# Kernel optimization log

Hardware: AMD Instinct MI355X
Metric: run time of the kernel (lower is better)

Reference implementation:

```python
import jax, jax.numpy as jnp
import numpy as np

B, F, D = 4096, 32, 32
LAYER_SIZE = [128, 128]


def setup_inputs() -> dict:
    key = jax.random.key(0)
    k1, k2, k3 = jax.random.split(key, 3)
    inputs = jax.random.normal(k1, (B, F, D), dtype=jnp.float32)
    # CIN filters: shape [1, field_nums[0]*field_nums[i], field_nums[i+1]]
    field_nums = [F] + LAYER_SIZE
    filter_0 = (jax.random.normal(k2, (1, field_nums[0] * field_nums[0], field_nums[1]), dtype=jnp.float32) * 0.05)
    filter_1 = (jax.random.normal(k3, (1, field_nums[0] * field_nums[1], field_nums[2]), dtype=jnp.float32) * 0.05)
    return {"inputs": inputs, "filter_0": filter_0, "filter_1": filter_1}


def _cin_forward(inputs, filters):
    x0 = inputs          # [B, F, D] -- hidden_nn_layers[0]
    prev = inputs        # hidden_nn_layers[-1]
    outs = []
    for W in filters:    # W: [1, F*M, N]
        # outer product over field dims: [B, F, M, D]
        z = jnp.einsum('bhd,bmd->bhmd', x0, prev)
        b, h, m, d = z.shape
        z = z.reshape(b, h * m, d)                 # [B, F*M, D]
        # 1x1 conv over the F*M axis == contraction with W[0]: [F*M, N]
        cur = jnp.einsum('bpd,pn->bnd', z, W[0])   # [B, N, D]
        cur = jax.nn.relu(cur)
        prev = cur
        outs.append(cur)
    result = jnp.concatenate(outs, axis=1)         # [B, sum(layer_size), D]
    return jnp.sum(result, axis=-1)                # [B, sum(layer_size)]


def reference(inputs, filter_0, filter_1):
    return _cin_forward(inputs, (filter_0, filter_1))
```

## Files before the change

kernel.cpp:

```cpp
#include <hip/hip_runtime.h>


typedef _Float16 half_t;
typedef _Float16 half4v __attribute__((ext_vector_type(4)));
typedef _Float16 half8 __attribute__((ext_vector_type(8)));
typedef float f32x16 __attribute__((ext_vector_type(16)));

__global__ void prep_w_kernel(const float* __restrict__ W0,
                              const float* __restrict__ W1,
                              half_t* __restrict__ Wp0,
                              half_t* __restrict__ Wp1) {
  int gid = blockIdx.x * 256 + threadIdx.x;
  int n = gid & 127;
  int tg = (gid >> 7) & 1;
  int s = gid >> 8;
  const float* W;
  half_t* Wp;
  int M, sl;
  if (s < 64) { W = W0; Wp = Wp0; M = 32; sl = s; }
  else        { W = W1; Wp = Wp1; M = 128; sl = s - 64; }
  int h = sl & 31, mc = sl >> 5;
  int kbase = h * M + mc * 16 + tg * 8;
  half8 v;
#pragma unroll
  for (int j = 0; j < 8; ++j) v[j] = (half_t)W[(size_t)(kbase + j) * 128 + n];
  *(half8*)(Wp + ((size_t)(sl * 2 + tg) * 128 + n) * 8) = v;
}

__device__ __forceinline__ int pswz(int row, int m) {
  return row * 128 + (((m >> 3) ^ (row & 15)) << 3) + (m & 7);
}

__device__ __forceinline__ f32x16 mfma3216(half8 a, half8 b, f32x16 c) {
  return __builtin_amdgcn_mfma_f32_32x32x16_f16(a, b, c, 0, 0, 0);
}

template <int MC, bool L1>
__device__ __forceinline__ void layer_loop(const half_t* __restrict__ Wp,
                                           const half_t* __restrict__ psrc,
                                           const half_t* __restrict__ xQb,
                                           int woff, int l31, int hi,
                                           f32x16 acc[8]) {
  half8 P[8];
#pragma unroll
  for (int rt = 0; rt < 8; ++rt)
    P[rt] = L1 ? *(const half8*)&psrc[(rt * 32 + l31) * 40 + hi * 8]
               : *(const half8*)&psrc[pswz(rt * 32 + l31, hi * 8)];

  half8 Br0 = *(const half8*)(Wp + (size_t)0 * 2048 + woff);
  half8 Br1 = *(const half8*)(Wp + (size_t)1 * 2048 + woff);
  half8 Br2 = *(const half8*)(Wp + (size_t)2 * 2048 + woff);
  half8 Br3 = *(const half8*)(Wp + (size_t)3 * 2048 + woff);

#pragma unroll 1
  for (int mc = 0; mc < MC; ++mc) {
#pragma unroll 1
    for (int p = 0; p < 8; ++p) {
      const int h0 = p * 4;
      const int sb = mc * 32 + h0;
      half8 xq0 = *(const half8*)(xQb + (h0 + 0) * 256);
      half8 xq1 = *(const half8*)(xQb + (h0 + 1) * 256);
      half8 xq2 = *(const half8*)(xQb + (h0 + 2) * 256);
      half8 xq3 = *(const half8*)(xQb + (h0 + 3) * 256);

#define SSTEP(XQ, BR, OFFJ)                                               \
  {                                                                       \
    half8 A0 = P[0] * XQ[0], A1 = P[1] * XQ[1], A2 = P[2] * XQ[2],        \
          A3 = P[3] * XQ[3];                                              \
    acc[0] = mfma3216(A0, BR, acc[0]);                                    \
    acc[1] = mfma3216(A1, BR, acc[1]);                                    \
    acc[2] = mfma3216(A2, BR, acc[2]);                                    \
    acc[3] = mfma3216(A3, BR, acc[3]);                                    \
    half8 A4 = P[4] * XQ[4], A5 = P[5] * XQ[5], A6 = P[6] * XQ[6],        \
          A7 = P[7] * XQ[7];                                              \
    acc[4] = mfma3216(A4, BR, acc[4]);                                    \
    acc[5] = mfma3216(A5, BR, acc[5]);                                    \
    acc[6] = mfma3216(A6, BR, acc[6]);                                    \
    acc[7] = mfma3216(A7, BR, acc[7]);                                    \
    BR = *(const half8*)(Wp +                                             \
                         (size_t)((sb + 4 + OFFJ) & (MC * 32 - 1)) * 2048 \
                         + woff);                                         \
  }
      SSTEP(xq0, Br0, 0)
      SSTEP(xq1, Br1, 1)
      SSTEP(xq2, Br2, 2)
      SSTEP(xq3, Br3, 3)
#undef SSTEP
    }
    if (mc + 1 < MC) {
      const int mn = (mc + 1) * 16;
#pragma unroll
      for (int rt = 0; rt < 8; ++rt)
        P[rt] = L1 ? *(const half8*)&psrc[(rt * 32 + l31) * 40 + mn + hi * 8]
                   : *(const half8*)&psrc[pswz(rt * 32 + l31, mn + hi * 8)];
    }
  }
}

__global__ __launch_bounds__(256, 2) void cin_fused_kernel(
    const float* __restrict__ x0,
    const half_t* __restrict__ Wp0,
    const half_t* __restrict__ Wp1,
    float* __restrict__ out) {
  __shared__ half_t xQ[32 * 32 * 8];
  __shared__ half_t prevT[8 * 32 * 128];
  half_t* xT = prevT;

  const int tid = threadIdx.x;
  const int b0 = blockIdx.x * 8;

  const float4* x4 = (const float4*)(x0 + (size_t)b0 * 1024);
#pragma unroll
  for (int r = 0; r < 8; ++r) {
    int q = r * 256 + tid;
    float4 v = x4[q];
    int e4 = q * 4;
    int bi = e4 >> 10, h = (e4 >> 5) & 31, d0 = e4 & 31;
    half4v hv = {(half_t)v.x, (half_t)v.y, (half_t)v.z, (half_t)v.w};
#pragma unroll
    for (int j = 0; j < 4; ++j) {
      xQ[(h * 32 + d0 + j) * 8 + bi] = hv[j];
      xT[(bi * 32 + d0 + j) * 40 + h] = hv[j];
    }
  }
  __syncthreads();

  const int lane = tid & 63;
  const int l31 = lane & 31;
  const int hi = lane >> 5;
  const int wave = tid >> 6;

  const int woff = hi * 1024 + (wave * 32 + l31) * 8;
  const half_t* xQb = xQ + l31 * 8;

  f32x16 acc[8];
#pragma unroll
  for (int rt = 0; rt < 8; ++rt)
#pragma unroll
    for (int r = 0; r < 16; ++r) acc[rt][r] = 0.f;

  layer_loop<2, true>(Wp0, xT, xQb, woff, l31, hi, acc);

  __syncthreads();

#pragma unroll
  for (int rt = 0; rt < 8; ++rt) {
    float s = 0.f;
#pragma unroll
    for (int r = 0; r < 16; ++r) {
      float v = acc[rt][r];
      v = v > 0.f ? v : 0.f;
      s += v;
      int d = (r & 3) + ((r >> 2) << 3) + hi * 4;
      prevT[pswz(rt * 32 + d, wave * 32 + l31)] = (half_t)v;
      acc[rt][r] = 0.f;
    }
    s += __shfl_down(s, 32);
    if (lane < 32)
      out[(size_t)(b0 + rt) * 256 + wave * 32 + lane] = s;
  }
  __syncthreads();

  layer_loop<8, false>(Wp1, prevT, xQb, woff, l31, hi, acc);

#pragma unroll
  for (int rt = 0; rt < 8; ++rt) {
    float s = 0.f;
#pragma unroll
    for (int r = 0; r < 16; ++r) {
      float v = acc[rt][r];
      s += v > 0.f ? v : 0.f;
    }
    s += __shfl_down(s, 32);
    if (lane < 32)
      out[(size_t)(b0 + rt) * 256 + 128 + wave * 32 + lane] = s;
  }
}

extern "C" void kernel_launch(void* const* d_in, const int* in_sizes, int n_in,
                              void* d_out, int out_size, void* d_ws,
                              size_t ws_size, hipStream_t stream) {
  const float* x0 = (const float*)d_in[0];
  const float* w0 = (const float*)d_in[1];
  const float* w1 = (const float*)d_in[2];
  float* out = (float*)d_out;
  char* ws = (char*)d_ws;

  half_t* Wp0 = (half_t*)(ws);
  half_t* Wp1 = (half_t*)(ws + 64 * 2048 * 2);

  hipLaunchKernelGGL(prep_w_kernel, dim3(320), dim3(256), 0, stream, w0, w1,
                     Wp0, Wp1);
  hipLaunchKernelGGL(cin_fused_kernel, dim3(512), dim3(256), 0, stream, x0,
                     Wp0, Wp1, out);
}
```

Before: 204.1 us.

## Shrink per-block batch tile from 8 to 2 samples and raise occupancy

Each block now processes 2 batch rows instead of 8, with 4x more blocks and a launch bound targeting 4 blocks per CU. The xQ shared layout is repacked so one half8 load supplies the x0 values for four fields across both batch rows. This cuts registers and LDS per block to improve occupancy and latency hiding. The cost is 4x less reuse of each loaded weight fragment, so global/L2 weight traffic per MFMA rises sharply.

```diff
diff --git a/kernel.cpp b/kernel.cpp
--- a/kernel.cpp
+++ b/kernel.cpp
@@ -40,12 +40,12 @@
                                            const half_t* __restrict__ psrc,
                                            const half_t* __restrict__ xQb,
                                            int woff, int l31, int hi,
-                                           f32x16 acc[8]) {
-  half8 P[8];
+                                           f32x16 acc[2]) {
+  half8 P[2];
 #pragma unroll
-  for (int rt = 0; rt < 8; ++rt)
-    P[rt] = L1 ? *(const half8*)&psrc[(rt * 32 + l31) * 40 + hi * 8]
-               : *(const half8*)&psrc[pswz(rt * 32 + l31, hi * 8)];
+  for (int bi = 0; bi < 2; ++bi)
+    P[bi] = L1 ? *(const half8*)&psrc[(bi * 32 + l31) * 40 + hi * 8]
+               : *(const half8*)&psrc[pswz(bi * 32 + l31, hi * 8)];
 
   half8 Br0 = *(const half8*)(Wp + (size_t)0 * 2048 + woff);
   half8 Br1 = *(const half8*)(Wp + (size_t)1 * 2048 + woff);
@@ -56,62 +56,50 @@
   for (int mc = 0; mc < MC; ++mc) {
 #pragma unroll 1
     for (int p = 0; p < 8; ++p) {
-      const int h0 = p * 4;
-      const int sb = mc * 32 + h0;
-      half8 xq0 = *(const half8*)(xQb + (h0 + 0) * 256);
-      half8 xq1 = *(const half8*)(xQb + (h0 + 1) * 256);
-      half8 xq2 = *(const half8*)(xQb + (h0 + 2) * 256);
-      half8 xq3 = *(const half8*)(xQb + (h0 + 3) * 256);
+      const int sb = mc * 32 + 4 * p;
+      half8 xq = *(const half8*)(xQb + p * 256);
 
-#define SSTEP(XQ, BR, OFFJ)                                               \
-  {                                                                       \
-    half8 A0 = P[0] * XQ[0], A1 = P[1] * XQ[1], A2 = P[2] * XQ[2],        \
-          A3 = P[3] * XQ[3];                                              \
-    acc[0] = mfma3216(A0, BR, acc[0]);                                    \
-    acc[1] = mfma3216(A1, BR, acc[1]);                                    \
-    acc[2] = mfma3216(A2, BR, acc[2]);                                    \
-    acc[3] = mfma3216(A3, BR, acc[3]);                                    \
-    half8 A4 = P[4] * XQ[4], A5 = P[5] * XQ[5], A6 = P[6] * XQ[6],        \
-          A7 = P[7] * XQ[7];                                              \
-    acc[4] = mfma3216(A4, BR, acc[4]);                                    \
-    acc[5] = mfma3216(A5, BR, acc[5]);                                    \
-    acc[6] = mfma3216(A6, BR, acc[6]);                                    \
-    acc[7] = mfma3216(A7, BR, acc[7]);                                    \
-    BR = *(const half8*)(Wp +                                             \
-                         (size_t)((sb + 4 + OFFJ) & (MC * 32 - 1)) * 2048 \
-                         + woff);                                         \
+#define SSTEP(J, BR)                                                       \
+  {                                                                        \
+    half8 A0 = P[0] * xq[J * 2 + 0];                                       \
+    half8 A1 = P[1] * xq[J * 2 + 1];                                       \
+    acc[0] = mfma3216(A0, BR, acc[0]);                                     \
+    acc[1] = mfma3216(A1, BR, acc[1]);                                     \
+    BR = *(const half8*)(Wp +                                              \
+                         (size_t)((sb + 4 + J) & (MC * 32 - 1)) * 2048 +   \
+                         woff);                                            \
   }
-      SSTEP(xq0, Br0, 0)
-      SSTEP(xq1, Br1, 1)
-      SSTEP(xq2, Br2, 2)
-      SSTEP(xq3, Br3, 3)
+      SSTEP(0, Br0)
+      SSTEP(1, Br1)
+      SSTEP(2, Br2)
+      SSTEP(3, Br3)
 #undef SSTEP
     }
     if (mc + 1 < MC) {
       const int mn = (mc + 1) * 16;
 #pragma unroll
-      for (int rt = 0; rt < 8; ++rt)
-        P[rt] = L1 ? *(const half8*)&psrc[(rt * 32 + l31) * 40 + mn + hi * 8]
-                   : *(const half8*)&psrc[pswz(rt * 32 + l31, mn + hi * 8)];
+      for (int bi = 0; bi < 2; ++bi)
+        P[bi] = L1 ? *(const half8*)&psrc[(bi * 32 + l31) * 40 + mn + hi * 8]
+                   : *(const half8*)&psrc[pswz(bi * 32 + l31, mn + hi * 8)];
     }
   }
 }
 
-__global__ __launch_bounds__(256, 2) void cin_fused_kernel(
+__global__ __launch_bounds__(256, 4) void cin_fused_kernel(
     const float* __restrict__ x0,
     const half_t* __restrict__ Wp0,
     const half_t* __restrict__ Wp1,
     float* __restrict__ out) {
-  __shared__ half_t xQ[32 * 32 * 8];
-  __shared__ half_t prevT[8 * 32 * 128];
+  __shared__ half_t xQ[8 * 32 * 8];
+  __shared__ half_t prevT[2 * 32 * 128];
   half_t* xT = prevT;
 
   const int tid = threadIdx.x;
-  const int b0 = blockIdx.x * 8;
+  const int b0 = blockIdx.x * 2;
 
   const float4* x4 = (const float4*)(x0 + (size_t)b0 * 1024);
 #pragma unroll
-  for (int r = 0; r < 8; ++r) {
+  for (int r = 0; r < 2; ++r) {
     int q = r * 256 + tid;
     float4 v = x4[q];
     int e4 = q * 4;
@@ -119,7 +107,7 @@
     half4v hv = {(half_t)v.x, (half_t)v.y, (half_t)v.z, (half_t)v.w};
 #pragma unroll
     for (int j = 0; j < 4; ++j) {
-      xQ[(h * 32 + d0 + j) * 8 + bi] = hv[j];
+      xQ[((h >> 2) * 32 + d0 + j) * 8 + (h & 3) * 2 + bi] = hv[j];
       xT[(bi * 32 + d0 + j) * 40 + h] = hv[j];
     }
   }
@@ -133,47 +121,47 @@
   const int woff = hi * 1024 + (wave * 32 + l31) * 8;
   const half_t* xQb = xQ + l31 * 8;
 
-  f32x16 acc[8];
+  f32x16 acc[2];
 #pragma unroll
-  for (int rt = 0; rt < 8; ++rt)
+  for (int bi = 0; bi < 2; ++bi)
 #pragma unroll
-    for (int r = 0; r < 16; ++r) acc[rt][r] = 0.f;
+    for (int r = 0; r < 16; ++r) acc[bi][r] = 0.f;
 
   layer_loop<2, true>(Wp0, xT, xQb, woff, l31, hi, acc);
 
   __syncthreads();
 
 #pragma unroll
-  for (int rt = 0; rt < 8; ++rt) {
+  for (int bi = 0; bi < 2; ++bi) {
     float s = 0.f;
 #pragma unroll
     for (int r = 0; r < 16; ++r) {
-      float v = acc[rt][r];
+      float v = acc[bi][r];
       v = v > 0.f ? v : 0.f;
       s += v;
       int d = (r & 3) + ((r >> 2) << 3) + hi * 4;
-      prevT[pswz(rt * 32 + d, wave * 32 + l31)] = (half_t)v;
-      acc[rt][r] = 0.f;
+      prevT[pswz(bi * 32 + d, wave * 32 + l31)] = (half_t)v;
+      acc[bi][r] = 0.f;
     }
     s += __shfl_down(s, 32);
     if (lane < 32)
-      out[(size_t)(b0 + rt) * 256 + wave * 32 + lane] = s;
+      out[(size_t)(b0 + bi) * 256 + wave * 32 + lane] = s;
   }
   __syncthreads();
 
   layer_loop<8, false>(Wp1, prevT, xQb, woff, l31, hi, acc);
 
 #pragma unroll
-  for (int rt = 0; rt < 8; ++rt) {
+  for (int bi = 0; bi < 2; ++bi) {
     float s = 0.f;
 #pragma unroll
     for (int r = 0; r < 16; ++r) {
-      float v = acc[rt][r];
+      float v = acc[bi][r];
       s += v > 0.f ? v : 0.f;
     }
     s += __shfl_down(s, 32);
     if (lane < 32)
-      out[(size_t)(b0 + rt) * 256 + 128 + wave * 32 + lane] = s;
+      out[(size_t)(b0 + bi) * 256 + 128 + wave * 32 + lane] = s;
   }
 }
 
@@ -191,6 +179,6 @@
 
   hipLaunchKernelGGL(prep_w_kernel, dim3(320), dim3(256), 0, stream, w0, w1,
                      Wp0, Wp1);
-  hipLaunchKernelGGL(cin_fused_kernel, dim3(512), dim3(256), 0, stream, x0,
+  hipLaunchKernelGGL(cin_fused_kernel, dim3(2048), dim3(256), 0, stream, x0,
                      Wp0, Wp1, out);
 }
```

Measured after the change: 231.1 us. 1.13x slower.
